# Performance work log

Measured on AMD Instinct MI355X. Metric: run time of the kernel, lower is better.

Reference implementation:

```python
import jax, jax.numpy as jnp
import numpy as np

T_VALUES = (4.0, 16.0, 64.0, 256.0)
EPS = 1e-05


def setup_inputs() -> dict:
    key = jax.random.key(0)
    k1, = jax.random.split(key, 1)
    B, F, T = 32, 128, 2000
    x = jax.random.uniform(k1, (B, F, T), dtype=jnp.float32)
    # learned log-parameters, initialized exactly like the torch module
    log_alpha = jnp.full((F,), jnp.log(0.8), dtype=jnp.float32)
    log_delta = jnp.full((F,), jnp.log(10.0), dtype=jnp.float32)
    log_r = jnp.full((F,), jnp.log(0.25), dtype=jnp.float32)
    return {"x": x, "log_alpha": log_alpha, "log_delta": log_delta, "log_r": log_r}


def _mrpcen(x, log_alpha, log_delta, log_r):
    # x: (B, F, T)
    t = jnp.asarray(T_VALUES, dtype=x.dtype)                      # (n_t,)
    s = (jnp.sqrt(1.0 + 4.0 * t ** 2) - 1.0) / (2.0 * t ** 2)     # (n_t,)
    s = s[:, None, None]                                          # (n_t,1,1)

    n_t = len(T_VALUES)
    B, F, T = x.shape
    xt = jnp.moveaxis(x, -1, 0)                                   # (T, B, F)
    m0 = jnp.broadcast_to(xt[0], (n_t, B, F))                     # (n_t, B, F)

    def step(m, x_frame):
        m_new = (1.0 - s) * m + s * x_frame                        # (n_t,B,F)
        return m_new, m_new

    _, ms = jax.lax.scan(step, m0, xt[1:])                        # (T-1, n_t, B, F)
    M = jnp.concatenate([m0[None], ms], axis=0)                   # (T, n_t, B, F)
    M = jnp.moveaxis(M, 0, -1)                                    # (n_t, B, F, T)

    alpha = jnp.exp(log_alpha)[:, None]                           # (F,1)
    delta = jnp.exp(log_delta)[:, None]                           # (F,1)
    r = jnp.exp(log_r)[:, None]                                   # (F,1)

    eps = jnp.asarray(EPS, dtype=x.dtype)
    smooth = jnp.exp(-alpha * (jnp.log(eps) + jnp.log1p(M / eps)))  # (n_t,B,F,T)
    pcen = (x[None] * smooth + delta) ** r - delta ** r             # (n_t,B,F,T)
    return jnp.transpose(pcen, (1, 0, 2, 3))                        # (B,n_t,F,T)


def reference(x, log_alpha, log_delta, log_r):
    return _mrpcen(x, log_alpha, log_delta, log_r)
```

## Files before the change

kernel.cpp:

```cpp
#include <hip/hip_runtime.h>


#define NT    4
#define TLEN  2000
#define FDIM  128
#define CHUNK 32
#define WPB   4

__global__ __launch_bounds__(256) void mrpcen_kernel(
    const float* __restrict__ x,
    const float* __restrict__ log_alpha,
    const float* __restrict__ log_delta,
    const float* __restrict__ log_r,
    float* __restrict__ out,
    int rows)
{
    const int w    = threadIdx.x >> 6;
    const int lane = threadIdx.x & 63;
    const int row  = blockIdx.x * WPB + w;
    if (row >= rows) return;
    const int b = row >> 7;
    const int f = row & (FDIM - 1);

    float xr[CHUNK];
    const float* xrow = x + (size_t)row * TLEN;
    const int base = lane * CHUNK;
#pragma unroll
    for (int q = 0; q < CHUNK / 4; ++q) {
        int pos = base + q * 4;
        float4 v = (pos < TLEN) ? ((const float4*)xrow)[pos >> 2]
                                : make_float4(0.f, 0.f, 0.f, 0.f);
        xr[q * 4 + 0] = v.x; xr[q * 4 + 1] = v.y;
        xr[q * 4 + 2] = v.z; xr[q * 4 + 3] = v.w;
    }

    const float alpha = __expf(log_alpha[f]);
    const float delta = __expf(log_delta[f]);
    const float rr    = __expf(log_r[f]);
    const float dr    = exp2f(rr * log2f(delta));
    const float eps   = 1e-5f;
    const float nalpha = -alpha;

    const float tvals[NT] = {4.f, 16.f, 64.f, 256.f};

#pragma unroll 1
    for (int ti = 0; ti < NT; ++ti) {
        const float t  = tvals[ti];
        const float s  = (sqrtf(1.f + 4.f * t * t) - 1.f) / (2.f * t * t);
        const float cs = 1.f - s;

        float c2  = cs * cs, c4 = c2 * c2, c8 = c4 * c4;
        float c16 = c8 * c8, c32 = c16 * c16;
        float A = (lane == 0) ? 0.f : (lane < 62) ? c32 : (lane == 62) ? c16 : 1.f;

        float B = 0.f;
#pragma unroll
        for (int j = 0; j < CHUNK; ++j) {
            int pos  = base + j;
            float a  = (pos < TLEN) ? cs : 1.0f;
            float bb = (pos < TLEN) ? s * xr[j] : 0.0f;
            if (pos == 0) { a = 0.0f; bb = xr[j]; }
            B = fmaf(a, B, bb);
        }

#pragma unroll
        for (int off = 1; off < 64; off <<= 1) {
            float Ap = __shfl_up(A, off, 64);
            float Bp = __shfl_up(B, off, 64);
            if (lane >= off) {
                B = fmaf(A, Bp, B);
                A = A * Ap;
            }
        }
        float m = __shfl_up(B, 1, 64);

        float* gout = out + ((size_t)(b * NT + ti) * FDIM + f) * TLEN;
        float o4[4];
#pragma unroll
        for (int j = 0; j < CHUNK; ++j) {
            int pos  = base + j;
            float a  = (pos < TLEN) ? cs : 1.0f;
            float bb = (pos < TLEN) ? s * xr[j] : 0.0f;
            if (pos == 0) { a = 0.0f; bb = xr[j]; }
            m = fmaf(a, m, bb);
            float smooth = exp2f(nalpha * log2f(eps + m));
            float v      = fmaf(xr[j], smooth, delta);
            o4[j & 3]    = exp2f(rr * log2f(v)) - dr;
            if ((j & 3) == 3) {
                int p0 = base + (j & ~3);
                if (p0 < TLEN)
                    ((float4*)gout)[p0 >> 2] =
                        make_float4(o4[0], o4[1], o4[2], o4[3]);
            }
        }
    }
}

extern "C" void kernel_launch(void* const* d_in, const int* in_sizes, int n_in,
                              void* d_out, int out_size, void* d_ws, size_t ws_size,
                              hipStream_t stream) {
    const float* x  = (const float*)d_in[0];
    const float* la = (const float*)d_in[1];
    const float* ld = (const float*)d_in[2];
    const float* lr = (const float*)d_in[3];
    float* out = (float*)d_out;

    const int rows   = in_sizes[0] / TLEN;
    const int blocks = (rows + WPB - 1) / WPB;
    hipLaunchKernelGGL(mrpcen_kernel, dim3(blocks), dim3(256), 0, stream,
                       x, la, ld, lr, out, rows);
}
```

Baseline: 196.0 us.

## Split time constants across waves and stage outputs in LDS for coalesced stores

Each wave now handles one (batch, feature, time-constant) output row instead of looping over all four time constants, giving four times more waves. Each row's outputs are first written to padded shared memory, then stored to global memory as contiguous float4 runs across lanes. This replaces the earlier strided per-lane float4 stores. Per-element boundary predicates in the scan loops are removed, which relies on zero-padded tail lanes whose outputs are never stored. The cost is reading x four times, served from cache, and extra LDS traffic.

After: 172.4 us. 12.0% less time.

```diff
diff --git a/kernel.cpp b/kernel.cpp
--- a/kernel.cpp
+++ b/kernel.cpp
@@ -1,29 +1,34 @@
 #include <hip/hip_runtime.h>
 
 
-#define NT    4
-#define TLEN  2000
-#define FDIM  128
-#define CHUNK 32
-#define WPB   4
+#define NT      4
+#define TLEN    2000
+#define FDIM    128
+#define CHUNK   32
+#define LSTRIDE 33
+#define ROWPAD  (64 * LSTRIDE)
+#define WPB     4
 
-__global__ __launch_bounds__(256) void mrpcen_kernel(
+__global__ __launch_bounds__(256, 4) void mrpcen_kernel(
     const float* __restrict__ x,
     const float* __restrict__ log_alpha,
     const float* __restrict__ log_delta,
     const float* __restrict__ log_r,
     float* __restrict__ out,
-    int rows)
+    int nrows)
 {
+    __shared__ float stage[WPB][ROWPAD];
+
     const int w    = threadIdx.x >> 6;
     const int lane = threadIdx.x & 63;
-    const int row  = blockIdx.x * WPB + w;
-    if (row >= rows) return;
-    const int b = row >> 7;
-    const int f = row & (FDIM - 1);
+    const int row2 = blockIdx.x * WPB + w;
+    if (row2 >= nrows) return;
+    const int f  = row2 & (FDIM - 1);
+    const int ti = (row2 >> 7) & (NT - 1);
+    const int b  = row2 >> 9;
 
     float xr[CHUNK];
-    const float* xrow = x + (size_t)row * TLEN;
+    const float* xrow = x + (size_t)(b * FDIM + f) * TLEN;
     const int base = lane * CHUNK;
 #pragma unroll
     for (int q = 0; q < CHUNK / 4; ++q) {
@@ -38,60 +43,50 @@
     const float delta = __expf(log_delta[f]);
     const float rr    = __expf(log_r[f]);
     const float dr    = exp2f(rr * log2f(delta));
+    const float nal   = -alpha;
     const float eps   = 1e-5f;
-    const float nalpha = -alpha;
 
-    const float tvals[NT] = {4.f, 16.f, 64.f, 256.f};
+    const float tv = (ti == 0) ? 4.f : (ti == 1) ? 16.f : (ti == 2) ? 64.f : 256.f;
+    const float s  = (sqrtf(1.f + 4.f * tv * tv) - 1.f) / (2.f * tv * tv);
+    const float cs = 1.f - s;
 
-#pragma unroll 1
-    for (int ti = 0; ti < NT; ++ti) {
-        const float t  = tvals[ti];
-        const float s  = (sqrtf(1.f + 4.f * t * t) - 1.f) / (2.f * t * t);
-        const float cs = 1.f - s;
+    float c2 = cs * cs, c4 = c2 * c2, c8 = c4 * c4, c16 = c8 * c8, c32 = c16 * c16;
+    float A = (lane == 0) ? 0.f : c32;
 
-        float c2  = cs * cs, c4 = c2 * c2, c8 = c4 * c4;
-        float c16 = c8 * c8, c32 = c16 * c16;
-        float A = (lane == 0) ? 0.f : (lane < 62) ? c32 : (lane == 62) ? c16 : 1.f;
-
-        float B = 0.f;
+    float B = (lane == 0) ? xr[0] : s * xr[0];
 #pragma unroll
-        for (int j = 0; j < CHUNK; ++j) {
-            int pos  = base + j;
-            float a  = (pos < TLEN) ? cs : 1.0f;
-            float bb = (pos < TLEN) ? s * xr[j] : 0.0f;
-            if (pos == 0) { a = 0.0f; bb = xr[j]; }
-            B = fmaf(a, B, bb);
-        }
+    for (int j = 1; j < CHUNK; ++j)
+        B = fmaf(cs, B, s * xr[j]);
 
 #pragma unroll
-        for (int off = 1; off < 64; off <<= 1) {
-            float Ap = __shfl_up(A, off, 64);
-            float Bp = __shfl_up(B, off, 64);
-            if (lane >= off) {
-                B = fmaf(A, Bp, B);
-                A = A * Ap;
-            }
-        }
-        float m = __shfl_up(B, 1, 64);
+    for (int off = 1; off < 64; off <<= 1) {
+        float Ap = __shfl_up(A, off, 64);
+        float Bp = __shfl_up(B, off, 64);
+        if (lane >= off) { B = fmaf(A, Bp, B); A *= Ap; }
+    }
+    float m = __shfl_up(B, 1, 64);
+    if (lane == 0) m = xr[0];
 
-        float* gout = out + ((size_t)(b * NT + ti) * FDIM + f) * TLEN;
-        float o4[4];
 #pragma unroll
-        for (int j = 0; j < CHUNK; ++j) {
-            int pos  = base + j;
-            float a  = (pos < TLEN) ? cs : 1.0f;
-            float bb = (pos < TLEN) ? s * xr[j] : 0.0f;
-            if (pos == 0) { a = 0.0f; bb = xr[j]; }
-            m = fmaf(a, m, bb);
-            float smooth = exp2f(nalpha * log2f(eps + m));
-            float v      = fmaf(xr[j], smooth, delta);
-            o4[j & 3]    = exp2f(rr * log2f(v)) - dr;
-            if ((j & 3) == 3) {
-                int p0 = base + (j & ~3);
-                if (p0 < TLEN)
-                    ((float4*)gout)[p0 >> 2] =
-                        make_float4(o4[0], o4[1], o4[2], o4[3]);
-            }
+    for (int j = 0; j < CHUNK; ++j) {
+        m = fmaf(cs, m, s * xr[j]);
+        float smooth = exp2f(nal * log2f(eps + m));
+        float v      = fmaf(xr[j], smooth, delta);
+        stage[w][lane * LSTRIDE + j] = exp2f(rr * log2f(v)) - dr;
+    }
+    __syncthreads();
+
+    float* gout = out + (size_t)row2 * TLEN;
+#pragma unroll
+    for (int k = 0; k < 8; ++k) {
+        int p0 = k * 256 + lane * 4;
+        if (p0 < TLEN) {
+            int r = p0 >> 5, c = p0 & 31;
+            float a0 = stage[w][r * LSTRIDE + c + 0];
+            float a1 = stage[w][r * LSTRIDE + c + 1];
+            float a2 = stage[w][r * LSTRIDE + c + 2];
+            float a3 = stage[w][r * LSTRIDE + c + 3];
+            ((float4*)gout)[p0 >> 2] = make_float4(a0, a1, a2, a3);
         }
     }
 }
@@ -105,8 +100,8 @@
     const float* lr = (const float*)d_in[3];
     float* out = (float*)d_out;
 
-    const int rows   = in_sizes[0] / TLEN;
-    const int blocks = (rows + WPB - 1) / WPB;
+    const int nrows  = out_size / TLEN;
+    const int blocks = (nrows + WPB - 1) / WPB;
     hipLaunchKernelGGL(mrpcen_kernel, dim3(blocks), dim3(256), 0, stream,
-                       x, la, ld, lr, out, rows);
+                       x, la, ld, lr, out, nrows);
 }
```
